# Kernel optimization log

Measured on AMD Instinct MI355X. Metric: run time of the kernel, lower is better.

## Reference

```python
import jax, jax.numpy as jnp
import numpy as np

IN_CH = 512; OUT_CH = 512; NOISE_SIZE = 512; K = 3; A = 0.2
B = 4; H = 32
_G = float(np.sqrt(2.0 / (1.0 + A * A)))                 # leaky_relu gain, a=0.2
CONV_SCALE = _G / float(np.sqrt(IN_CH * K * K))          # equal-lr kaiming scale (fan_in = in_ch*3*3)
MS_SCALE = float(np.sqrt(2.0 / (NOISE_SIZE + IN_CH)))    # equal-lr xavier scale on make_s linear
RGB_SCALE = _G * float(np.sqrt(2.0 / (OUT_CH + 3)))      # equal-lr xavier scale on 1x1 to_rgb


def upsample2x(x):
    # torch F.interpolate(scale_factor=2, mode='bilinear', align_corners=False)
    b, c, h, w = x.shape
    return jax.image.resize(x, (b, c, 2 * h, 2 * w), method='bilinear')


def mod_conv(x, style, weight, bias, ms_w, ms_b, w_scale, demodulate, pad):
    # style -> per-sample input-channel scales s: (B, Cin)
    s = style @ (ms_w.T * MS_SCALE) + ms_b
    Wmod = (weight * w_scale)[None] * s[:, None, :, None, None]   # (B, Cout, Cin, k, k)
    if demodulate:
        d = jax.lax.rsqrt(jnp.sum(Wmod * Wmod, axis=(2, 3, 4)) + 1e-8)
        Wmod = Wmod * d[:, :, None, None, None]
    conv1 = lambda xi, wi: jax.lax.conv_general_dilated(
        xi[None], wi, (1, 1), [(pad, pad), (pad, pad)],
        dimension_numbers=('NCHW', 'OIHW', 'NCHW'))[0]
    y = jax.vmap(conv1)(x, Wmod)                                   # per-sample weights == grouped conv
    return y + bias[None, :, None, None]


def lrelu(x):
    return jnp.where(x >= 0, x, A * x)


def setup_inputs() -> dict:
    key = jax.random.key(0)
    ks = jax.random.split(key, 19)
    r = lambda i, shape: jax.random.normal(ks[i], shape, dtype=jnp.float32)
    return {
        'maps': r(0, (B, IN_CH, H, H)),
        'w': r(1, (B, NOISE_SIZE)),
        'rgb': r(2, (B, 3, H, H)),
        'noise0': r(3, (B, 1, 2 * H, 2 * H)),
        'noise1': r(4, (B, 1, 2 * H, 2 * H)),
        'conv0_w': r(5, (OUT_CH, IN_CH, K, K)),
        'conv0_b': 0.1 * r(6, (OUT_CH,)),
        'ms0_w': r(7, (IN_CH, NOISE_SIZE)),
        'ms0_b': jnp.ones((IN_CH,), jnp.float32),
        'ns0': 0.1 * r(8, (OUT_CH,)),
        'conv1_w': r(9, (OUT_CH, OUT_CH, K, K)),
        'conv1_b': 0.1 * r(10, (OUT_CH,)),
        'ms1_w': r(11, (OUT_CH, NOISE_SIZE)),
        'ms1_b': jnp.ones((OUT_CH,), jnp.float32),
        'ns1': 0.1 * r(12, (OUT_CH,)),
        'rgb_w': r(13, (3, OUT_CH, 1, 1)),
        'rgb_b': 0.1 * r(14, (3,)),
        'msr_w': r(15, (OUT_CH, NOISE_SIZE)),
        'msr_b': jnp.ones((OUT_CH,), jnp.float32),
    }


def reference(maps, w, rgb, noise0, noise1,
              conv0_w, conv0_b, ms0_w, ms0_b, ns0,
              conv1_w, conv1_b, ms1_w, ms1_b, ns1,
              rgb_w, rgb_b, msr_w, msr_b):
    # upsample branch (upsample=True)
    rgb = upsample2x(rgb)
    maps = upsample2x(maps)
    # layer 0: modulated conv -> noise -> leaky relu
    h = mod_conv(maps, w, conv0_w, conv0_b, ms0_w, ms0_b, CONV_SCALE, True, 1)
    h = lrelu(h + ns0[None, :, None, None] * noise0)
    # layer 1
    h = mod_conv(h, w, conv1_w, conv1_b, ms1_w, ms1_b, CONV_SCALE, True, 1)
    h = lrelu(h + ns1[None, :, None, None] * noise1)
    # to_rgb: 1x1 modulated conv, no demodulation
    rgb_out = rgb + mod_conv(h, w, rgb_w, rgb_b, msr_w, msr_b, RGB_SCALE, False, 0)
    return (rgb_out, h)
```

## Files before the change

kernel.cpp:

```cpp
#include <hip/hip_runtime.h>
#include <stdint.h>


#define BATCH 4
#define CH 512
#define NPP 4356
#define HOUT_OFF 49152

static constexpr double G_GAIN = 1.3867504905630728;
static constexpr float CONV_SCALE_F = (float)(G_GAIN / 67.88225099390857);
static constexpr float MS_SCALE_F = 0.044194173824159216f;
static constexpr float RGB_SCALE_F = (float)(G_GAIN * 1.4142135623730951 / 22.693611435820433);

typedef __attribute__((ext_vector_type(8))) short short8;
typedef __attribute__((ext_vector_type(4))) float floatx4;

#define OFF_FLAG   0
#define OFF_S0     256
#define OFF_S1     (OFF_S0 + 8192)
#define OFF_SR     (OFF_S1 + 8192)
#define OFF_D0     (OFF_SR + 8192)
#define OFF_D1     (OFF_D0 + 8192)
#define OFF_B0F    (OFF_D1 + 8192)
#define OFF_B1F    (OFF_B0F + 2048)
#define OFF_NS0F   (OFF_B1F + 2048)
#define OFF_NS1F   (OFF_NS0F + 2048)
#define OFF_RGBBF  (OFF_NS1F + 2048)
#define OFF_WMODR  (OFF_RGBBF + 256)
#define OFF_N0F    (OFF_WMODR + 24576)
#define OFF_N1F    (OFF_N0F + 65536)
#define OFF_WT0    (OFF_N1F + 65536)
#define WT_BYTES   4718592
#define OFF_WT1    (OFF_WT0 + WT_BYTES)
#define OFF_XP0    (OFF_WT1 + WT_BYTES)
#define XP_BYTES   17842176
#define OFF_XP1    (OFF_XP0 + XP_BYTES)

__device__ __forceinline__ float bf2f(unsigned short u) {
  return __uint_as_float(((unsigned int)u) << 16);
}
__device__ __forceinline__ unsigned short f2bf(float f) {
  unsigned int x = __float_as_uint(f);
  unsigned int r = x + 0x7FFFu + ((x >> 16) & 1u);
  return (unsigned short)(r >> 16);
}
__device__ __forceinline__ float ldin(const void* p, long i, int bf) {
  if (bf) return bf2f(((const unsigned short*)p)[i]);
  return ((const float*)p)[i];
}
__device__ __forceinline__ void async_ld16(const void* g, void* l) {
  __builtin_amdgcn_global_load_lds(
      (const __attribute__((address_space(1))) unsigned int*)g,
      (__attribute__((address_space(3))) unsigned int*)l, 16, 0, 0);
}
__device__ __forceinline__ void upw(int o, int n_in, int& lo, int& hi, float& wlo) {
  int k = o >> 1;
  if (o & 1) { lo = k; hi = k + 1; if (hi > n_in - 1) hi = n_in - 1; wlo = 0.75f; }
  else       { lo = k - 1; if (lo < 0) lo = 0; hi = k; wlo = 0.25f; }
}

__global__ void k_flag(const unsigned int* msb, int* flag) {
  if (threadIdx.x == 0 && blockIdx.x == 0)
    *flag = (msb[0] == 0x3F803F80u) ? 1 : 0;
}

__global__ void k_zero(unsigned short* Xp) {
  const int idx = blockIdx.x * 256 + threadIdx.x;
  const int plane = idx / 132;
  const int rem = idx - plane * 132;
  const int row65 = rem >= 66;
  const int col = rem - (row65 ? 66 : 0);
  const short8 z = {0, 0, 0, 0, 0, 0, 0, 0};
  *(short8*)&Xp[((long)plane * NPP + (row65 ? 65 : 0) * 66 + col) * 8] = z;
}

__global__ void k_styles(const void* w, const void* msw0, const void* msb0,
                         const void* msw1, const void* msb1,
                         const void* mswr, const void* msbr,
                         float* s0, float* s1, float* sr, const int* flagp) {
  const int bf = *flagp;
  const int mat = blockIdx.x >> 7, chunk = blockIdx.x & 127;
  const int wv = threadIdx.x >> 6, lane = threadIdx.x & 63;
  const int i = chunk * 4 + wv;
  const void* msw; const void* msb; float* out;
  if (mat == 0)      { msw = msw0; msb = msb0; out = s0; }
  else if (mat == 1) { msw = msw1; msb = msb1; out = s1; }
  else               { msw = mswr; msb = msbr; out = sr; }
  float a[4] = {0.f, 0.f, 0.f, 0.f};
  const int n0 = lane * 8;
  if (bf) {
    short8 m8 = *(const short8*)((const unsigned short*)msw + (long)i * 512 + n0);
    for (int b = 0; b < 4; ++b) {
      short8 w8 = *(const short8*)((const unsigned short*)w + b * 512 + n0);
      float s = 0.f;
      for (int e = 0; e < 8; ++e)
        s += bf2f((unsigned short)m8[e]) * bf2f((unsigned short)w8[e]);
      a[b] = s;
    }
  } else {
    const float* mrow = (const float*)msw + (long)i * 512 + n0;
    float4 m0v = *(const float4*)mrow, m1v = *(const float4*)(mrow + 4);
    for (int b = 0; b < 4; ++b) {
      const float* wr = (const float*)w + b * 512 + n0;
      float4 w0v = *(const float4*)wr, w1v = *(const float4*)(wr + 4);
      a[b] = m0v.x * w0v.x + m0v.y * w0v.y + m0v.z * w0v.z + m0v.w * w0v.w +
             m1v.x * w1v.x + m1v.y * w1v.y + m1v.z * w1v.z + m1v.w * w1v.w;
    }
  }
  for (int off = 1; off < 64; off <<= 1)
    for (int b = 0; b < 4; ++b) a[b] += __shfl_xor(a[b], off, 64);
  if (lane == 0) {
    const float mb = ldin(msb, i, bf);
    for (int b = 0; b < 4; ++b) out[b * 512 + i] = a[b] * MS_SCALE_F + mb;
  }
}

__global__ void k_convert(const void* b0, const void* b1, const void* nv0, const void* nv1,
                          const void* rb, const void* rw, const void* noise0, const void* noise1,
                          float* ob0, float* ob1, float* ons0, float* ons1, float* orb,
                          float* owmr, float* on0, float* on1,
                          const float* sr, const int* flagp) {
  const int bf = *flagp;
  const int t = blockIdx.x * blockDim.x + threadIdx.x;
  const int stride = gridDim.x * blockDim.x;
  if (t < 512) {
    ob0[t] = ldin(b0, t, bf); ob1[t] = ldin(b1, t, bf);
    ons0[t] = ldin(nv0, t, bf); ons1[t] = ldin(nv1, t, bf);
  }
  if (t < 3) orb[t] = ldin(rb, t, bf);
  for (int i = t; i < 16384; i += stride) {
    on0[i] = ldin(noise0, i, bf);
    on1[i] = ldin(noise1, i, bf);
  }
  for (int i = t; i < 4 * 3 * 512; i += stride) {
    int b = i / 1536; int r = i - b * 1536; int c = r >> 9; int ci = r & 511;
    owmr[i] = RGB_SCALE_F * ldin(rw, c * 512 + ci, bf) * sr[b * 512 + ci];
  }
}

__global__ void k_wtd(const void* w0, const void* w1, const float* s0, const float* s1,
                      unsigned short* Wt0, unsigned short* Wt1,
                      float* S0, float* S1, const int* flagp) {
  const int bf = *flagp;
  const int l = blockIdx.x >> 9, co = blockIdx.x & 511;
  const void* w = l ? w1 : w0;
  const float* s = l ? s1 : s0;
  unsigned short* Wt = l ? Wt1 : Wt0;
  float* S = l ? S1 : S0;
  float part[4] = {0.f, 0.f, 0.f, 0.f};
  for (int h = 0; h < 2; ++h) {
    const int ci = threadIdx.x + h * 256;
    const int kb = ci >> 5, q = (ci >> 3) & 3, j = ci & 7;
    const long rbase = ((long)co * 512 + ci) * 9;
    float wsq = 0.f;
    for (int t = 0; t < 9; ++t) {
      float v = ldin(w, rbase + t, bf);
      wsq += v * v;
      Wt[((((long)t * 16 + kb) * 4 + q) * 512 + co) * 8 + j] = f2bf(v);
    }
    for (int b = 0; b < 4; ++b) {
      float sv = s[b * 512 + ci];
      part[b] += sv * sv * wsq;
    }
  }
  __shared__ float red[256 * 4];
  for (int b = 0; b < 4; ++b) red[threadIdx.x * 4 + b] = part[b];
  __syncthreads();
  for (int off = 128; off > 0; off >>= 1) {
    if (threadIdx.x < off)
      for (int b = 0; b < 4; ++b)
        red[threadIdx.x * 4 + b] += red[(threadIdx.x + off) * 4 + b];
    __syncthreads();
  }
  if (threadIdx.x < 4) S[threadIdx.x * 512 + co] = red[threadIdx.x];
}

__global__ void k_upt(const void* maps, const float* s0, unsigned short* Xp0,
                      const int* flagp) {
  const int bf = *flagp;
  const int t = blockIdx.x, kb = blockIdx.y, b = blockIdx.z;
  __shared__ float lds[32][4][32];
  {
    const int ciq = threadIdx.x >> 5;
    const int x = threadIdx.x & 31;
    for (int cc = 0; cc < 4; ++cc) {
      const int ci = cc * 8 + ciq;
      const long cbase = ((long)(b * 512 + kb * 32 + ci)) << 10;
      for (int r = 0; r < 4; ++r) {
        int ir = 2 * t - 1 + r;
        ir = ir < 0 ? 0 : (ir > 31 ? 31 : ir);
        lds[ci][r][x] = ldin(maps, cbase + ir * 32 + x, bf);
      }
    }
  }
  __syncthreads();
  const int q = threadIdx.x >> 6, px = threadIdx.x & 63;
  int xlo, xhi; float wx;
  upw(px, 32, xlo, xhi, wx);
  float sv[8];
  for (int jj = 0; jj < 8; ++jj) sv[jj] = s0[b * 512 + kb * 32 + q * 8 + jj];
  for (int y = 0; y < 4; ++y) {
    const int yg = 4 * t + y;
    int ylo, yhi; float wy;
    upw(yg, 32, ylo, yhi, wy);
    const int rlo = ylo - (2 * t - 1), rhi = yhi - (2 * t - 1);
    short8 pk;
    for (int jj = 0; jj < 8; ++jj) {
      const int ci = q * 8 + jj;
      float vlo = wx * lds[ci][rlo][xlo] + (1.f - wx) * lds[ci][rlo][xhi];
      float vhi = wx * lds[ci][rhi][xlo] + (1.f - wx) * lds[ci][rhi][xhi];
      float v = (wy * vlo + (1.f - wy) * vhi) * sv[jj];
      pk[jj] = (short)f2bf(v);
    }
    *(short8*)&Xp0[((((long)b * 16 + kb) * 4 + q) * NPP + (yg + 1) * 66 + (px + 1)) * 8] = pk;
  }
}

#define MFMA16 __builtin_amdgcn_mfma_f32_16x16x32_bf16
template <int LAYER>
__global__ __launch_bounds__(256, 2) void k_conv(
    const unsigned short* __restrict__ Wt,
    const unsigned short* Xp,
    const float* __restrict__ Ssum,
    const float* __restrict__ bias,
    const float* __restrict__ nsc,
    const float* __restrict__ noise,
    const float* __restrict__ snext,
    unsigned short* XpOut,
    void* dout,
    const int* __restrict__ flagp) {
  __shared__ __align__(16) unsigned short Al[2][12288];
  __shared__ __align__(16) unsigned short Bl[8192];
  const int mt = blockIdx.x & 3, nt = blockIdx.x >> 2, b = blockIdx.y;
  const int m0 = mt << 7, y0 = nt << 1;
  const int lane = threadIdx.x & 63, wv = threadIdx.x >> 6;
  const int wm = wv >> 1, wn = wv & 1;
  const int q = lane >> 4, l15 = lane & 15;
  const int q1 = wv >> 1, hh = wv & 1;

  const floatx4 vz = {0.f, 0.f, 0.f, 0.f};
  floatx4 c00 = vz, c01 = vz, c02 = vz, c03 = vz;
  floatx4 c10 = vz, c11 = vz, c12 = vz, c13 = vz;
  floatx4 c20 = vz, c21 = vz, c22 = vz, c23 = vz;
  floatx4 c30 = vz, c31 = vz, c32 = vz, c33 = vz;

  auto issueA = [&](int kb, int ky, int bu) {
    for (int s = 0; s < 6; ++s) {
      const int kx = s >> 1;
      const int qq = q1 + ((s & 1) << 1);
      const unsigned short* src =
          Wt + ((((long)(ky * 3 + kx) * 16 + kb) * 4 + qq) * 512 + m0 + hh * 64 + lane) * 8;
      async_ld16(src, &Al[bu][((qq * 3 + kx) * 128 + hh * 64) * 8]);
    }
  };
  auto issueB2 = [&](int kb, int r0) {
    for (int r = 0; r < 2; ++r) {
      const int row = r0 + r;
      const unsigned short* src =
          Xp + ((((long)b * 16 + kb) * 4 + wv) * NPP + (long)(y0 + row) * 66 + 1 + lane) * 8;
      async_ld16(src, &Bl[((row * 4 + wv) * 64) * 8]);
    }
  };

  issueA(0, 0, 0);
  issueB2(0, 0);

  const short8 z8 = {0, 0, 0, 0, 0, 0, 0, 0};
  int buf = 0;
#pragma unroll 1
  for (int kb = 0; kb < 16; ++kb) {
    for (int ky = 0; ky < 3; ++ky) {
      __syncthreads();
      {
        int kyn = ky + 1, kbn = kb;
        if (kyn == 3) { kyn = 0; kbn = kb + 1; if (kbn == 16) kbn = 0; }
        issueA(kbn, kyn, buf ^ 1);
        if (ky == 0) issueB2(kb, 2);
        else if (ky == 2) issueB2(kb + 1 == 16 ? 0 : kb + 1, 0);
      }
      const unsigned short* Ab = &Al[buf][0];
      const int sq = ((wn + ky) * 4 + q) * 64;
#define TAPC(KX)                                                               \
  {                                                                            \
    const unsigned short* ap = Ab + ((q * 3 + (KX)) * 128 + wm * 64 + l15) * 8;\
    short8 aa0 = *(const short8*)(ap);                                         \
    short8 aa1 = *(const short8*)(ap + 128);                                   \
    short8 aa2 = *(const short8*)(ap + 256);                                   \
    short8 aa3 = *(const short8*)(ap + 384);                                   \
    short8 bb0, bb1, bb2, bb3;                                                 \
    {                                                                          \
      int p = 0 * 16 + l15 + (KX);                                             \
      int pc = p < 1 ? 0 : p - 1;                                              \
      bb0 = *(const short8*)&Bl[(sq + pc) * 8];                                \
      if ((KX) == 0) bb0 = (p == 0) ? z8 : bb0;                                \
    }                                                                          \
    bb1 = *(const short8*)&Bl[(sq + 1 * 16 + l15 + (KX)-1) * 8];               \
    bb2 = *(const short8*)&Bl[(sq + 2 * 16 + l15 + (KX)-1) * 8];               \
    {                                                                          \
      int p = 3 * 16 + l15 + (KX);                                             \
      int pc = p > 64 ? 63 : p - 1;                                            \
      bb3 = *(const short8*)&Bl[(sq + pc) * 8];                                \
      if ((KX) == 2) bb3 = (p == 65) ? z8 : bb3;                               \
    }                                                                          \
    c00 = MFMA16(aa0, bb0, c00, 0, 0, 0); c01 = MFMA16(aa0, bb1, c01, 0, 0, 0);\
    c02 = MFMA16(aa0, bb2, c02, 0, 0, 0); c03 = MFMA16(aa0, bb3, c03, 0, 0, 0);\
    c10 = MFMA16(aa1, bb0, c10, 0, 0, 0); c11 = MFMA16(aa1, bb1, c11, 0, 0, 0);\
    c12 = MFMA16(aa1, bb2, c12, 0, 0, 0); c13 = MFMA16(aa1, bb3, c13, 0, 0, 0);\
    c20 = MFMA16(aa2, bb0, c20, 0, 0, 0); c21 = MFMA16(aa2, bb1, c21, 0, 0, 0);\
    c22 = MFMA16(aa2, bb2, c22, 0, 0, 0); c23 = MFMA16(aa2, bb3, c23, 0, 0, 0);\
    c30 = MFMA16(aa3, bb0, c30, 0, 0, 0); c31 = MFMA16(aa3, bb1, c31, 0, 0, 0);\
    c32 = MFMA16(aa3, bb2, c32, 0, 0, 0); c33 = MFMA16(aa3, bb3, c33, 0, 0, 0);\
  }
      TAPC(0)
      TAPC(1)
      TAPC(2)
#undef TAPC
      buf ^= 1;
    }
  }

  floatx4 accv[4][4] = {{c00, c01, c02, c03}, {c10, c11, c12, c13},
                        {c20, c21, c22, c23}, {c30, c31, c32, c33}};
  const int bfflag = *flagp;
  const int coB = m0 + (wm << 6) + ((lane >> 4) << 2);
  const int xB = lane & 15;
  const int y = y0 + wn;
  for (int i = 0; i < 4; ++i) {
    const int co = coB + (i << 4);
    float Ds[4], bi[4], nv[4], sx[4];
    for (int r = 0; r < 4; ++r) {
      float Sv = Ssum[b * 512 + co + r];
      Ds[r] = CONV_SCALE_F * rsqrtf(CONV_SCALE_F * CONV_SCALE_F * Sv + 1e-8f);
      bi[r] = bias[co + r];
      nv[r] = nsc[co + r];
      sx[r] = (LAYER == 0) ? snext[b * 512 + co + r] : 0.f;
    }
    for (int j = 0; j < 4; ++j) {
      const int x = (j << 4) + xB;
      const int p = (y << 6) + x;
      const float nz = noise[b * 4096 + p];
      if (LAYER == 0) {
        unsigned long long pk = 0ull;
        for (int r = 0; r < 4; ++r) {
          float v = accv[i][j][r] * Ds[r] + bi[r] + nv[r] * nz;
          v = (v >= 0.f) ? v : 0.2f * v;
          pk |= (unsigned long long)f2bf(v * sx[r]) << (16 * r);
        }
        const int pp = (y + 1) * 66 + (x + 1);
        const long o = ((((long)b * 16 + (co >> 5)) * 4 + ((co >> 3) & 3)) * NPP + pp) * 8 + (co & 7);
        *(unsigned long long*)(XpOut + o) = pk;
      } else {
        for (int r = 0; r < 4; ++r) {
          float v = accv[i][j][r] * Ds[r] + bi[r] + nv[r] * nz;
          v = (v >= 0.f) ? v : 0.2f * v;
          const long o = (((long)(b * 512 + co + r)) << 12) + p;
          if (bfflag) ((unsigned short*)dout)[HOUT_OFF + o] = f2bf(v);
          else        ((float*)dout)[HOUT_OFF + o] = v;
        }
      }
    }
  }
}

__global__ void k_rgb(const void* rgb_in, const float* wmodr, const float* rgbb,
                      void* dout, const int* flagp) {
  const int bf = *flagp;
  const int b = blockIdx.y, p0 = blockIdx.x * 64;
  const int px = threadIdx.x & 63, g = threadIdx.x >> 6;
  const char* hbytes = (const char*)dout + (long)HOUT_OFF * (bf ? 2 : 4);
  float a0 = 0.f, a1 = 0.f, a2 = 0.f;
  const float* wm = wmodr + b * 1536;
  for (int ci = g * 128; ci < g * 128 + 128; ++ci) {
    const long o = (((long)(b * 512 + ci)) << 12) + p0 + px;
    const float hv = bf ? bf2f(((const unsigned short*)hbytes)[o])
                        : ((const float*)hbytes)[o];
    a0 += wm[ci] * hv;
    a1 += wm[512 + ci] * hv;
    a2 += wm[1024 + ci] * hv;
  }
  __shared__ float red[4][3][64];
  red[g][0][px] = a0; red[g][1][px] = a1; red[g][2][px] = a2;
  __syncthreads();
  if (g == 0) {
    const int p = p0 + px;
    const int y = p >> 6, x = p & 63;
    int ylo, yhi, xlo, xhi; float wy, wx;
    upw(y, 32, ylo, yhi, wy);
    upw(x, 32, xlo, xhi, wx);
    for (int c = 0; c < 3; ++c) {
      float s = red[0][c][px] + red[1][c][px] + red[2][c][px] + red[3][c][px];
      const long base = (long)(b * 3 + c) << 10;
      const float v00 = ldin(rgb_in, base + ylo * 32 + xlo, bf);
      const float v01 = ldin(rgb_in, base + ylo * 32 + xhi, bf);
      const float v10 = ldin(rgb_in, base + yhi * 32 + xlo, bf);
      const float v11 = ldin(rgb_in, base + yhi * 32 + xhi, bf);
      const float up = wy * (wx * v00 + (1.f - wx) * v01) +
                       (1.f - wy) * (wx * v10 + (1.f - wx) * v11);
      const float v = up + s + rgbb[c];
      const long o = ((long)(b * 3 + c) << 12) + p;
      if (bf) ((unsigned short*)dout)[o] = f2bf(v);
      else    ((float*)dout)[o] = v;
    }
  }
}

extern "C" void kernel_launch(void* const* d_in, const int* in_sizes, int n_in,
                              void* d_out, int out_size, void* d_ws, size_t ws_size,
                              hipStream_t stream) {
  char* ws = (char*)d_ws;
  int* flag = (int*)(ws + OFF_FLAG);
  float* s0 = (float*)(ws + OFF_S0);
  float* s1 = (float*)(ws + OFF_S1);
  float* sr = (float*)(ws + OFF_SR);
  float* S0 = (float*)(ws + OFF_D0);
  float* S1 = (float*)(ws + OFF_D1);
  float* b0f = (float*)(ws + OFF_B0F);
  float* b1f = (float*)(ws + OFF_B1F);
  float* ns0f = (float*)(ws + OFF_NS0F);
  float* ns1f = (float*)(ws + OFF_NS1F);
  float* rgbbf = (float*)(ws + OFF_RGBBF);
  float* wmodr = (float*)(ws + OFF_WMODR);
  float* n0f = (float*)(ws + OFF_N0F);
  float* n1f = (float*)(ws + OFF_N1F);
  unsigned short* Wt0 = (unsigned short*)(ws + OFF_WT0);
  unsigned short* Wt1 = (unsigned short*)(ws + OFF_WT1);
  unsigned short* Xp0 = (unsigned short*)(ws + OFF_XP0);
  unsigned short* Xp1 = (unsigned short*)(ws + OFF_XP1);

  k_flag<<<1, 64, 0, stream>>>((const unsigned int*)d_in[8], flag);
  k_zero<<<264, 256, 0, stream>>>(Xp0);
  k_styles<<<384, 256, 0, stream>>>(d_in[1], d_in[7], d_in[8], d_in[12], d_in[13],
                                    d_in[17], d_in[18], s0, s1, sr, flag);
  k_convert<<<64, 256, 0, stream>>>(d_in[6], d_in[11], d_in[9], d_in[14], d_in[16],
                                    d_in[15], d_in[3], d_in[4], b0f, b1f, ns0f, ns1f,
                                    rgbbf, wmodr, n0f, n1f, sr, flag);
  k_wtd<<<1024, 256, 0, stream>>>(d_in[5], d_in[10], s0, s1, Wt0, Wt1, S0, S1, flag);
  k_upt<<<dim3(16, 16, 4), 256, 0, stream>>>(d_in[0], s0, Xp0, flag);
  k_conv<0><<<dim3(128, 4), 256, 0, stream>>>(Wt0, Xp0, S0, b0f, ns0f, n0f, s1, Xp1,
                                              d_out, flag);
  k_conv<1><<<dim3(128, 4), 256, 0, stream>>>(Wt1, Xp1, S1, b1f, ns1f, n1f, s1, Xp1,
                                              d_out, flag);
  k_rgb<<<dim3(64, 4), 256, 0, stream>>>(d_in[2], wmodr, rgbbf, d_out, flag);
  (void)in_sizes; (void)n_in; (void)out_size; (void)ws_size;
}
```

Before: 308.9 us.

## Load conv weight fragments directly from global into registers, drop LDS A staging

```diff
diff --git a/kernel.cpp b/kernel.cpp
--- a/kernel.cpp
+++ b/kernel.cpp
@@ -229,14 +229,13 @@
     unsigned short* XpOut,
     void* dout,
     const int* __restrict__ flagp) {
-  __shared__ __align__(16) unsigned short Al[2][12288];
   __shared__ __align__(16) unsigned short Bl[8192];
-  const int mt = blockIdx.x & 3, nt = blockIdx.x >> 2, b = blockIdx.y;
+  const int idx = blockIdx.x;
+  const int mt = idx & 3, b = (idx >> 2) & 3, nt = idx >> 4;
   const int m0 = mt << 7, y0 = nt << 1;
   const int lane = threadIdx.x & 63, wv = threadIdx.x >> 6;
   const int wm = wv >> 1, wn = wv & 1;
   const int q = lane >> 4, l15 = lane & 15;
-  const int q1 = wv >> 1, hh = wv & 1;
 
   const floatx4 vz = {0.f, 0.f, 0.f, 0.f};
   floatx4 c00 = vz, c01 = vz, c02 = vz, c03 = vz;
@@ -244,15 +243,8 @@
   floatx4 c20 = vz, c21 = vz, c22 = vz, c23 = vz;
   floatx4 c30 = vz, c31 = vz, c32 = vz, c33 = vz;
 
-  auto issueA = [&](int kb, int ky, int bu) {
-    for (int s = 0; s < 6; ++s) {
-      const int kx = s >> 1;
-      const int qq = q1 + ((s & 1) << 1);
-      const unsigned short* src =
-          Wt + ((((long)(ky * 3 + kx) * 16 + kb) * 4 + qq) * 512 + m0 + hh * 64 + lane) * 8;
-      async_ld16(src, &Al[bu][((qq * 3 + kx) * 128 + hh * 64) * 8]);
-    }
-  };
+  const unsigned short* Wbase = Wt + ((long)q * 512 + m0 + wm * 64 + l15) * 8;
+
   auto issueB2 = [&](int kb, int r0) {
     for (int r = 0; r < 2; ++r) {
       const int row = r0 + r;
@@ -262,31 +254,28 @@
     }
   };
 
-  issueA(0, 0, 0);
   issueB2(0, 0);
 
   const short8 z8 = {0, 0, 0, 0, 0, 0, 0, 0};
-  int buf = 0;
 #pragma unroll 1
   for (int kb = 0; kb < 16; ++kb) {
+#pragma unroll 1
     for (int ky = 0; ky < 3; ++ky) {
+      short8 a_[3][4];
+#pragma unroll
+      for (int kx = 0; kx < 3; ++kx) {
+        const unsigned short* ap = Wbase + ((long)((ky * 3 + kx) * 16 + kb) * 4) * 512 * 8;
+#pragma unroll
+        for (int i = 0; i < 4; ++i)
+          a_[kx][i] = *(const short8*)(ap + i * 128);
+      }
       __syncthreads();
-      {
-        int kyn = ky + 1, kbn = kb;
-        if (kyn == 3) { kyn = 0; kbn = kb + 1; if (kbn == 16) kbn = 0; }
-        issueA(kbn, kyn, buf ^ 1);
-        if (ky == 0) issueB2(kb, 2);
-        else if (ky == 2) issueB2(kb + 1 == 16 ? 0 : kb + 1, 0);
-      }
-      const unsigned short* Ab = &Al[buf][0];
+      if (ky == 0) issueB2(kb, 2);
+      else if (ky == 2) issueB2(kb + 1 == 16 ? 0 : kb + 1, 0);
       const int sq = ((wn + ky) * 4 + q) * 64;
 #define TAPC(KX)                                                               \
   {                                                                            \
-    const unsigned short* ap = Ab + ((q * 3 + (KX)) * 128 + wm * 64 + l15) * 8;\
-    short8 aa0 = *(const short8*)(ap);                                         \
-    short8 aa1 = *(const short8*)(ap + 128);                                   \
-    short8 aa2 = *(const short8*)(ap + 256);                                   \
-    short8 aa3 = *(const short8*)(ap + 384);                                   \
+    short8 aa0 = a_[KX][0], aa1 = a_[KX][1], aa2 = a_[KX][2], aa3 = a_[KX][3]; \
     short8 bb0, bb1, bb2, bb3;                                                 \
     {                                                                          \
       int p = 0 * 16 + l15 + (KX);                                             \
@@ -315,7 +304,6 @@
       TAPC(1)
       TAPC(2)
 #undef TAPC
-      buf ^= 1;
     }
   }
 
@@ -436,10 +424,10 @@
                                     rgbbf, wmodr, n0f, n1f, sr, flag);
   k_wtd<<<1024, 256, 0, stream>>>(d_in[5], d_in[10], s0, s1, Wt0, Wt1, S0, S1, flag);
   k_upt<<<dim3(16, 16, 4), 256, 0, stream>>>(d_in[0], s0, Xp0, flag);
-  k_conv<0><<<dim3(128, 4), 256, 0, stream>>>(Wt0, Xp0, S0, b0f, ns0f, n0f, s1, Xp1,
-                                              d_out, flag);
-  k_conv<1><<<dim3(128, 4), 256, 0, stream>>>(Wt1, Xp1, S1, b1f, ns1f, n1f, s1, Xp1,
-                                              d_out, flag);
+  k_conv<0><<<512, 256, 0, stream>>>(Wt0, Xp0, S0, b0f, ns0f, n0f, s1, Xp1,
+                                     d_out, flag);
+  k_conv<1><<<512, 256, 0, stream>>>(Wt1, Xp1, S1, b1f, ns1f, n1f, s1, Xp1,
+                                     d_out, flag);
   k_rgb<<<dim3(64, 4), 256, 0, stream>>>(d_in[2], wmodr, rgbbf, d_out, flag);
   (void)in_sizes; (void)n_in; (void)out_size; (void)ws_size;
 }
```

Result: faster. 295.3 us (-4.4%).
